# Kernel tuning notes

Hardware: AMD Instinct MI355X
Metric: run time of the kernel (lower is better)

## Reference

```python
import jax, jax.numpy as jnp
import numpy as np

N = 50000      # nodes
E = 800000     # edges (before self-loops)
D = 128        # hid_d
H = 8          # heads
C = D // H     # per-head channels
L = 3          # layers
SLOPE = 0.2    # GATv2 leaky_relu negative slope
EPS = 1e-5     # LayerNorm eps


def setup_inputs() -> dict:
    key = jax.random.key(0)
    ks = jax.random.split(key, 8)
    x = jax.random.normal(ks[0], (N, D), dtype=jnp.float32)
    ei = jax.random.randint(ks[1], (2, E), 0, N, dtype=jnp.int32)
    s = 1.0 / np.sqrt(D)
    Wl = jax.random.normal(ks[2], (L, D, D), dtype=jnp.float32) * s   # source transform per layer
    Wr = jax.random.normal(ks[3], (L, D, D), dtype=jnp.float32) * s   # target transform per layer
    att = jax.random.normal(ks[4], (L, H, C), dtype=jnp.float32) * (1.0 / np.sqrt(C))
    bias = jnp.zeros((L, D), dtype=jnp.float32)
    gamma = jnp.ones((L, D), dtype=jnp.float32)
    beta = jnp.zeros((L, D), dtype=jnp.float32)
    return {"x": x, "Wl": Wl, "Wr": Wr, "att": att, "bias": bias,
            "gamma": gamma, "beta": beta, "ei": ei}


def _layernorm(y, g, b):
    mu = jnp.mean(y, axis=-1, keepdims=True)
    var = jnp.mean(jnp.square(y - mu), axis=-1, keepdims=True)
    return (y - mu) * jax.lax.rsqrt(var + EPS) * g + b


def reference(x, Wl, Wr, att, bias, gamma, beta, ei):
    # append self-loops (PyG GATv2Conv default add_self_loops=True)
    loops = jnp.arange(N, dtype=ei.dtype)
    src = jnp.concatenate([ei[0], loops])  # [E+N]
    dst = jnp.concatenate([ei[1], loops])  # [E+N]
    h = x
    for l in range(L):
        xl = (h @ Wl[l]).reshape(N, H, C)   # source-side features
        xr = (h @ Wr[l]).reshape(N, H, C)   # target-side features
        feat = xl[src] + xr[dst]            # [E+N, H, C] per-edge gather
        logits = jnp.einsum('ehc,hc->eh', jax.nn.leaky_relu(feat, SLOPE), att[l])
        # segment softmax over incoming edges of each dst node
        m = jax.ops.segment_max(logits, dst, num_segments=N)
        ex = jnp.exp(logits - m[dst])
        denom = jax.ops.segment_sum(ex, dst, num_segments=N)
        alpha = ex / denom[dst]             # [E+N, H]
        msg = alpha[:, :, None] * xl[src]   # [E+N, H, C]
        out = jax.ops.segment_sum(msg, dst, num_segments=N).reshape(N, H * C) + bias[l]
        # wrapper: h = h + dropout(elu(norm(gat(h)))) ; dropout = identity (eval)
        h = h + jax.nn.elu(_layernorm(out, gamma[l], beta[l]))
    return h
```

## Files before the change

### kernel.cpp

```cpp
#include <hip/hip_runtime.h>
#include <hip/hip_fp16.h>
#include <math.h>

#define N_NODES 50000
#define N_EDGES 800000
#define D 128
#define L 3
#define SLOPE 0.2f
#define LN_EPS 1e-5f
#define ETOT (N_EDGES + N_NODES)
#define SCAN_BLOCKS ((N_NODES + 1023) / 1024)

typedef _Float16 half8 __attribute__((ext_vector_type(8)));
typedef _Float16 h4v  __attribute__((ext_vector_type(4)));
typedef _Float16 h2v  __attribute__((ext_vector_type(2)));
typedef float f32x4 __attribute__((ext_vector_type(4)));


__global__ void rank_hist_kernel(const int* __restrict__ ei, int* __restrict__ counts,
                                 int* __restrict__ rank) {
    int idx = blockIdx.x * blockDim.x + threadIdx.x;
    if (idx >= ETOT) return;
    int d = (idx < N_EDGES) ? ei[N_EDGES + idx] : (idx - N_EDGES);
    rank[idx] = atomicAdd(&counts[d], 1);
}

__global__ __launch_bounds__(1024) void scan1_kernel(const int* __restrict__ counts,
                                                     int* __restrict__ offsets,
                                                     int* __restrict__ bsum) {
    __shared__ int wsum[16];
    int tid = threadIdx.x;
    int lane = tid & 63, w = tid >> 6;
    int i = blockIdx.x * 1024 + tid;
    int v = (i < N_NODES) ? counts[i] : 0;
    int sc = v;
    #pragma unroll
    for (int off = 1; off < 64; off <<= 1) {
        int u = __shfl_up(sc, off);
        if (lane >= off) sc += u;
    }
    if (lane == 63) wsum[w] = sc;
    __syncthreads();
    if (w == 0) {
        int t2 = (lane < 16) ? wsum[lane] : 0;
        #pragma unroll
        for (int off = 1; off < 16; off <<= 1) {
            int u = __shfl_up(t2, off);
            if (lane >= off) t2 += u;
        }
        if (lane < 16) wsum[lane] = t2;
    }
    __syncthreads();
    int wpref = (w == 0) ? 0 : wsum[w - 1];
    if (i < N_NODES) offsets[i] = wpref + sc - v;
    if (tid == 0) bsum[blockIdx.x] = wsum[15];
}

__global__ __launch_bounds__(64) void scan2_kernel(const int* __restrict__ bsum,
                                                   int* __restrict__ bpre) {
    int lane = threadIdx.x;
    int v = (lane < SCAN_BLOCKS) ? bsum[lane] : 0;
    int sc = v;
    #pragma unroll
    for (int off = 1; off < 64; off <<= 1) {
        int u = __shfl_up(sc, off);
        if (lane >= off) sc += u;
    }
    if (lane < SCAN_BLOCKS) bpre[lane] = sc - v;
}

__global__ __launch_bounds__(1024) void scan3_kernel(int* __restrict__ offsets,
                                                     const int* __restrict__ bpre) {
    int i = blockIdx.x * 1024 + threadIdx.x;
    if (i < N_NODES) offsets[i] += bpre[blockIdx.x];
    if (i == 0) offsets[N_NODES] = ETOT;
}

__global__ void scatter_kernel(const int* __restrict__ ei, const int* __restrict__ offsets,
                               const int* __restrict__ rank,
                               unsigned short* __restrict__ sorted16) {
    int idx = blockIdx.x * blockDim.x + threadIdx.x;
    if (idx >= ETOT) return;
    int s, d;
    if (idx < N_EDGES) { s = ei[idx]; d = ei[N_EDGES + idx]; }
    else               { s = d = idx - N_EDGES; }
    sorted16[offsets[d] + rank[idx]] = (unsigned short)s;
}


__global__ __launch_bounds__(256) void wfrag_kernel(const float* __restrict__ Wl,
                                                    const float* __restrict__ Wr,
                                                    _Float16* __restrict__ Wfrag) {
    int u = blockIdx.x * 256 + threadIdx.x;
    if (u >= 3 * 4096) return;
    int lane = u & 63, nt = (u >> 6) & 7, kt = (u >> 9) & 3, y = (u >> 11) & 1, l = u >> 12;
    int r = lane & 15, q = lane >> 4;
    const float* W = (y ? Wr : Wl) + (size_t)l * D * D;
    half8 v;
    #pragma unroll
    for (int j = 0; j < 8; ++j)
        v[j] = (_Float16)W[(kt * 32 + q * 8 + j) * D + nt * 16 + r];
    *(half8*)&Wfrag[(size_t)u * 8] = v;
}


__global__ __launch_bounds__(256) void gemm_mfma_kernel(
        const float* __restrict__ h, const _Float16* __restrict__ WfragL,
        _Float16* __restrict__ xlh, _Float16* __restrict__ xrh) {
    __shared__ half8 Afrag[1024];
    int t = threadIdx.x;
    int row0 = blockIdx.x * 64;
    {
        int kt = t >> 6, q = (t >> 4) & 3, r = t & 15;
        int kc = kt * 4 + q;
        #pragma unroll
        for (int i = 0; i < 4; ++i) {
            int row = row0 + i * 16 + r;
            float4 f0 = make_float4(0.f, 0.f, 0.f, 0.f), f1 = f0;
            if (row < N_NODES) {
                const float* p = &h[(size_t)row * D + kc * 8];
                f0 = *(const float4*)p;
                f1 = *(const float4*)(p + 4);
            }
            half8 v;
            v[0] = (_Float16)f0.x; v[1] = (_Float16)f0.y;
            v[2] = (_Float16)f0.z; v[3] = (_Float16)f0.w;
            v[4] = (_Float16)f1.x; v[5] = (_Float16)f1.y;
            v[6] = (_Float16)f1.z; v[7] = (_Float16)f1.w;
            Afrag[i * 256 + t] = v;
        }
    }
    __syncthreads();
    int w = t >> 6, lane = t & 63;
    f32x4 acc[16];
    #pragma unroll
    for (int i = 0; i < 16; ++i) acc[i] = (f32x4){0.f, 0.f, 0.f, 0.f};
    #pragma unroll
    for (int kt = 0; kt < 4; ++kt) {
        half8 a = Afrag[(w * 4 + kt) * 64 + lane];
        #pragma unroll
        for (int y = 0; y < 2; ++y) {
            #pragma unroll
            for (int nt = 0; nt < 8; ++nt) {
                half8 b = *(const half8*)&WfragL[(size_t)(((y * 4 + kt) * 8 + nt) * 64 + lane) * 8];
                acc[y * 8 + nt] = __builtin_amdgcn_mfma_f32_16x16x32_f16(a, b, acc[y * 8 + nt], 0, 0, 0);
            }
        }
    }
    int rq = lane >> 4, rc = lane & 15;
    int rbase = row0 + w * 16 + rq * 4;
    #pragma unroll
    for (int y = 0; y < 2; ++y) {
        _Float16* out = y ? xrh : xlh;
        #pragma unroll
        for (int nt = 0; nt < 8; ++nt) {
            #pragma unroll
            for (int reg = 0; reg < 4; ++reg) {
                int row = rbase + reg;
                if (row < N_NODES)
                    out[(size_t)row * D + nt * 16 + rc] = (_Float16)acc[y * 8 + nt][reg];
            }
        }
    }
}


__device__ __forceinline__ float quad_reduce4(float p) {
    int t;
    t = __builtin_amdgcn_update_dpp(0, __float_as_int(p), 0xB1, 0xF, 0xF, true);
    p += __int_as_float(t);
    t = __builtin_amdgcn_update_dpp(0, __float_as_int(p), 0x4E, 0xF, 0xF, true);
    p += __int_as_float(t);
    return p;
}

__device__ __forceinline__ float logit4(h4v v, h2v xrA, h2v xrB, h2v attA, h2v attB,
                                        h2v slope2) {
    h2v v0; v0[0] = v[0]; v0[1] = v[1];
    h2v v1; v1[0] = v[2]; v1[1] = v[3];
    h2v f0 = v0 + xrA;
    h2v f1 = v1 + xrB;
    h2v lf0 = __builtin_elementwise_max(f0, f0 * slope2);
    h2v lf1 = __builtin_elementwise_max(f1, f1 * slope2);
    float p = __builtin_amdgcn_fdot2(lf0, attA, 0.f, false);
    return __builtin_amdgcn_fdot2(lf1, attB, p, false);
}

template<int KUN, bool MASK>
__device__ __forceinline__ void edge_block(
        int j, int idx_bp, unsigned off, unsigned laneoff, const char* xlb,
        h2v xrA, h2v xrB, h2v attA, h2v attB, h2v slope2, int cnt,
        float& s, float& a0, float& a1, float& a2, float& a3) {
    h4v vs[KUN];
    #pragma unroll
    for (int k = 0; k < KUN; ++k) {
        int o = __builtin_amdgcn_ds_bpermute(idx_bp + 4 * (j + k), (int)off);
        vs[k] = *(const h4v*)(xlb + ((unsigned)o + laneoff));
    }
    #pragma unroll
    for (int k = 0; k < KUN; ++k) {
        float p = logit4(vs[k], xrA, xrB, attA, attB, slope2);
        p = quad_reduce4(p);
        float e = __builtin_amdgcn_exp2f(p);
        if (MASK) e = (j + k < cnt) ? e : 0.f;
        s += e;
        a0 = fmaf(e, (float)vs[k][0], a0);
        a1 = fmaf(e, (float)vs[k][1], a1);
        a2 = fmaf(e, (float)vs[k][2], a2);
        a3 = fmaf(e, (float)vs[k][3], a3);
    }
}

__global__ __launch_bounds__(256) void gat_node_kernel(
        const _Float16* __restrict__ xlh, const _Float16* __restrict__ xrh,
        const int* __restrict__ offsets, const unsigned short* __restrict__ sorted16,
        const float* __restrict__ att_l, const float* __restrict__ bias_l,
        const float* __restrict__ gamma_l, const float* __restrict__ beta_l,
        const float* __restrict__ hin, float* __restrict__ hout) {
    int wid = (blockIdx.x * blockDim.x + threadIdx.x) >> 6;
    if (wid * 2 >= N_NODES) return;
    int lane = threadIdx.x & 63;
    int sub = lane >> 5, hl = lane & 31;
    int node = wid * 2 + sub;
    unsigned laneoff = hl * 8u;
    int idx_bp = sub << 7;

    h4v xr4 = *(const h4v*)&xrh[(size_t)node * D + hl * 4];
    h2v xrA; xrA[0] = xr4[0]; xrA[1] = xr4[1];
    h2v xrB; xrB[0] = xr4[2]; xrB[1] = xr4[3];
    float4 attf = *(const float4*)&att_l[hl * 4];
    h2v attA, attB, slope2;
    attA[0] = (_Float16)(attf.x * 1.44269504f);
    attA[1] = (_Float16)(attf.y * 1.44269504f);
    attB[0] = (_Float16)(attf.z * 1.44269504f);
    attB[1] = (_Float16)(attf.w * 1.44269504f);
    slope2[0] = (_Float16)SLOPE;
    slope2[1] = (_Float16)SLOPE;

    int beg = offsets[node], end = offsets[node + 1];
    int deg = end - beg;
    int degA = __builtin_amdgcn_readlane(deg, 0);
    int degB = __builtin_amdgcn_readlane(deg, 32);
    int degMax = degA > degB ? degA : degB;
    int degMin = degA < degB ? degA : degB;

    float s = 0.f;
    float acc0 = 0.f, acc1 = 0.f, acc2 = 0.f, acc3 = 0.f;
    const char* xlb = (const char*)xlh;

    for (int c0 = 0; c0 < degMax; c0 += 32) {
        int rem = deg - c0;
        int cnt = rem > 32 ? 32 : rem;
        int cl  = cnt > 0 ? (hl < cnt ? hl : cnt - 1) : 0;
        int pos = cnt > 0 ? beg + c0 + cl : beg;
        unsigned off = ((unsigned)sorted16[pos]) << 8;
        int jmax = degMax - c0; if (jmax > 32) jmax = 32;
        int nfull = degMin - c0; if (nfull > 32) nfull = 32; if (nfull < 0) nfull = 0;
        int j = 0;
        for (; j + 16 <= nfull; j += 16)
            edge_block<16, false>(j, idx_bp, off, laneoff, xlb, xrA, xrB,
                                  attA, attB, slope2, cnt, s, acc0, acc1, acc2, acc3);
        for (; j + 16 <= jmax; j += 16)
            edge_block<16, true>(j, idx_bp, off, laneoff, xlb, xrA, xrB,
                                 attA, attB, slope2, cnt, s, acc0, acc1, acc2, acc3);
        for (; j + 4 <= jmax; j += 4)
            edge_block<4, true>(j, idx_bp, off, laneoff, xlb, xrA, xrB,
                                attA, attB, slope2, cnt, s, acc0, acc1, acc2, acc3);
        for (; j < jmax; ++j)
            edge_block<1, true>(j, idx_bp, off, laneoff, xlb, xrA, xrB,
                                attA, attB, slope2, cnt, s, acc0, acc1, acc2, acc3);
    }

    float inv = 1.f / s;
    float4 bia = *(const float4*)&bias_l[hl * 4];
    float o0 = acc0 * inv + bia.x;
    float o1 = acc1 * inv + bia.y;
    float o2 = acc2 * inv + bia.z;
    float o3 = acc3 * inv + bia.w;
    float sum = (o0 + o1) + (o2 + o3);
    float sq  = (o0 * o0 + o1 * o1) + (o2 * o2 + o3 * o3);
    #pragma unroll
    for (int msk = 1; msk < 32; msk <<= 1) {
        sum += __shfl_xor(sum, msk);
        sq  += __shfl_xor(sq, msk);
    }
    float mu   = sum * (1.f / 128.f);
    float var  = sq * (1.f / 128.f) - mu * mu;
    float rstd = rsqrtf(var + LN_EPS);
    float4 gam = *(const float4*)&gamma_l[hl * 4];
    float4 bet = *(const float4*)&beta_l[hl * 4];
    float y0 = (o0 - mu) * rstd * gam.x + bet.x;
    float y1 = (o1 - mu) * rstd * gam.y + bet.y;
    float y2 = (o2 - mu) * rstd * gam.z + bet.z;
    float y3 = (o3 - mu) * rstd * gam.w + bet.w;
    y0 = y0 > 0.f ? y0 : __expf(y0) - 1.f;
    y1 = y1 > 0.f ? y1 : __expf(y1) - 1.f;
    y2 = y2 > 0.f ? y2 : __expf(y2) - 1.f;
    y3 = y3 > 0.f ? y3 : __expf(y3) - 1.f;
    size_t di = (size_t)node * D + hl * 4;
    float4 hv = *(const float4*)&hin[di];
    hv.x += y0; hv.y += y1; hv.z += y2; hv.w += y3;
    *(float4*)&hout[di] = hv;
}


extern "C" void kernel_launch(void* const* d_in, const int* in_sizes, int n_in,
                              void* d_out, int out_size, void* d_ws, size_t ws_size,
                              hipStream_t stream) {
    const float* x     = (const float*)d_in[0];
    const float* Wl    = (const float*)d_in[1];
    const float* Wr    = (const float*)d_in[2];
    const float* att   = (const float*)d_in[3];
    const float* bias  = (const float*)d_in[4];
    const float* gamma = (const float*)d_in[5];
    const float* beta  = (const float*)d_in[6];
    const int*   ei    = (const int*)d_in[7];
    float* h = (float*)d_out;

    char* ws = (char*)d_ws;
    _Float16* xlh = (_Float16*)ws;   ws += (size_t)N_NODES * D * sizeof(_Float16);
    _Float16* xrh = (_Float16*)ws;   ws += (size_t)N_NODES * D * sizeof(_Float16);
    _Float16* Wfrag = (_Float16*)ws; ws += (size_t)3 * 4096 * 8 * sizeof(_Float16);
    int* offsets = (int*)ws;         ws += (size_t)(N_NODES + 4) * sizeof(int);
    int* counts  = (int*)ws;         ws += (size_t)N_NODES * sizeof(int);
    int* bsum    = (int*)ws;         ws += 64 * sizeof(int);
    int* bpre    = (int*)ws;         ws += 64 * sizeof(int);
    int* rank    = (int*)ws;         ws += (size_t)ETOT * sizeof(int);
    unsigned short* sorted16 = (unsigned short*)ws;

    wfrag_kernel<<<48, 256, 0, stream>>>(Wl, Wr, Wfrag);
    (void)hipMemsetAsync(counts, 0, (size_t)N_NODES * sizeof(int), stream);
    rank_hist_kernel<<<(ETOT + 255) / 256, 256, 0, stream>>>(ei, counts, rank);
    scan1_kernel<<<SCAN_BLOCKS, 1024, 0, stream>>>(counts, offsets, bsum);
    scan2_kernel<<<1, 64, 0, stream>>>(bsum, bpre);
    scan3_kernel<<<SCAN_BLOCKS, 1024, 0, stream>>>(offsets, bpre);
    scatter_kernel<<<(ETOT + 255) / 256, 256, 0, stream>>>(ei, offsets, rank, sorted16);

    int gat_waves  = (N_NODES + 1) / 2;
    int gat_blocks = (gat_waves * 64 + 255) / 256;
    for (int l = 0; l < L; ++l) {
        const float* hin = (l == 0) ? x : h;
        gemm_mfma_kernel<<<(N_NODES + 63) / 64, 256, 0, stream>>>(
            hin, Wfrag + (size_t)l * 4096 * 8, xlh, xrh);
        gat_node_kernel<<<gat_blocks, 256, 0, stream>>>(
            xlh, xrh, offsets, sorted16,
            att + (size_t)l * D, bias + (size_t)l * D,
            gamma + (size_t)l * D, beta + (size_t)l * D, hin, h);
    }
}
```

Before: 336.6 us.

## Process four nodes per wave with 8-wide lanes and degree-sorted node order

The GAT aggregation kernel now assigns 16 lanes per node, with each lane handling 8 channels through half8 loads, so a wave covers four nodes. This also shortens the head reduction to a single DPP step. A counting sort by in-degree, built from a histogram, a scan and a scatter, produces a node permutation so that the four nodes sharing a wave have similar degrees, which cuts masked iterations from divergent degrees. In exchange it adds three small preprocessing kernels and a memset, and writes to hout in permuted, less coalesced order.

```diff
diff --git a/kernel.cpp b/kernel.cpp
--- a/kernel.cpp
+++ b/kernel.cpp
@@ -85,6 +85,43 @@
     if (idx < N_EDGES) { s = ei[idx]; d = ei[N_EDGES + idx]; }
     else               { s = d = idx - N_EDGES; }
     sorted16[offsets[d] + rank[idx]] = (unsigned short)s;
+}
+
+
+__global__ void deg_hist_kernel(const int* __restrict__ counts, int* __restrict__ hist) {
+    int i = blockIdx.x * blockDim.x + threadIdx.x;
+    if (i >= N_NODES) return;
+    int d = counts[i]; if (d > 255) d = 255;
+    atomicAdd(&hist[d], 1);
+}
+
+__global__ __launch_bounds__(64) void deg_scan_kernel(const int* __restrict__ hist,
+                                                      int* __restrict__ histoff) {
+    int lane = threadIdx.x;
+    int4 v = ((const int4*)hist)[lane];
+    int t = v.x + v.y + v.z + v.w;
+    int sc = t;
+    #pragma unroll
+    for (int off = 1; off < 64; off <<= 1) {
+        int u = __shfl_up(sc, off);
+        if (lane >= off) sc += u;
+    }
+    int base = sc - t;
+    int4 o;
+    o.x = base;
+    o.y = base + v.x;
+    o.z = base + v.x + v.y;
+    o.w = base + v.x + v.y + v.z;
+    ((int4*)histoff)[lane] = o;
+}
+
+__global__ void deg_scatter_kernel(const int* __restrict__ counts, int* __restrict__ histoff,
+                                   int* __restrict__ perm) {
+    int i = blockIdx.x * blockDim.x + threadIdx.x;
+    if (i >= N_NODES) return;
+    int d = counts[i]; if (d > 255) d = 255;
+    int pos = atomicAdd(&histoff[d], 1);
+    perm[pos] = i;
 }
 
 
@@ -165,142 +202,158 @@
 }
 
 
-__device__ __forceinline__ float quad_reduce4(float p) {
+__device__ __forceinline__ float pair_reduce2(float p) {
     int t;
     t = __builtin_amdgcn_update_dpp(0, __float_as_int(p), 0xB1, 0xF, 0xF, true);
     p += __int_as_float(t);
-    t = __builtin_amdgcn_update_dpp(0, __float_as_int(p), 0x4E, 0xF, 0xF, true);
-    p += __int_as_float(t);
     return p;
 }
 
-__device__ __forceinline__ float logit4(h4v v, h2v xrA, h2v xrB, h2v attA, h2v attB,
-                                        h2v slope2) {
-    h2v v0; v0[0] = v[0]; v0[1] = v[1];
-    h2v v1; v1[0] = v[2]; v1[1] = v[3];
-    h2v f0 = v0 + xrA;
-    h2v f1 = v1 + xrB;
-    h2v lf0 = __builtin_elementwise_max(f0, f0 * slope2);
-    h2v lf1 = __builtin_elementwise_max(f1, f1 * slope2);
-    float p = __builtin_amdgcn_fdot2(lf0, attA, 0.f, false);
-    return __builtin_amdgcn_fdot2(lf1, attB, p, false);
+__device__ __forceinline__ float logit8(half8 v, half8 xr, const h2v* att4, h2v slope2) {
+    float p = 0.f;
+    #pragma unroll
+    for (int i = 0; i < 4; ++i) {
+        h2v a; a[0] = v[2 * i];  a[1] = v[2 * i + 1];
+        h2v b; b[0] = xr[2 * i]; b[1] = xr[2 * i + 1];
+        h2v f  = a + b;
+        h2v lf = __builtin_elementwise_max(f, f * slope2);
+        p = __builtin_amdgcn_fdot2(lf, att4[i], p, false);
+    }
+    return p;
 }
 
 template<int KUN, bool MASK>
 __device__ __forceinline__ void edge_block(
         int j, int idx_bp, unsigned off, unsigned laneoff, const char* xlb,
-        h2v xrA, h2v xrB, h2v attA, h2v attB, h2v slope2, int cnt,
-        float& s, float& a0, float& a1, float& a2, float& a3) {
-    h4v vs[KUN];
+        half8 xr8, const h2v* att4, h2v slope2, int cnt,
+        float& s, float* acc) {
+    half8 vs[KUN];
     #pragma unroll
     for (int k = 0; k < KUN; ++k) {
         int o = __builtin_amdgcn_ds_bpermute(idx_bp + 4 * (j + k), (int)off);
-        vs[k] = *(const h4v*)(xlb + ((unsigned)o + laneoff));
+        vs[k] = *(const half8*)(xlb + ((unsigned)o + laneoff));
     }
     #pragma unroll
     for (int k = 0; k < KUN; ++k) {
-        float p = logit4(vs[k], xrA, xrB, attA, attB, slope2);
-        p = quad_reduce4(p);
+        float p = logit8(vs[k], xr8, att4, slope2);
+        p = pair_reduce2(p);
         float e = __builtin_amdgcn_exp2f(p);
         if (MASK) e = (j + k < cnt) ? e : 0.f;
         s += e;
-        a0 = fmaf(e, (float)vs[k][0], a0);
-        a1 = fmaf(e, (float)vs[k][1], a1);
-        a2 = fmaf(e, (float)vs[k][2], a2);
-        a3 = fmaf(e, (float)vs[k][3], a3);
+        #pragma unroll
+        for (int i = 0; i < 8; ++i)
+            acc[i] = fmaf(e, (float)vs[k][i], acc[i]);
     }
 }
 
 __global__ __launch_bounds__(256) void gat_node_kernel(
         const _Float16* __restrict__ xlh, const _Float16* __restrict__ xrh,
         const int* __restrict__ offsets, const unsigned short* __restrict__ sorted16,
+        const int* __restrict__ perm,
         const float* __restrict__ att_l, const float* __restrict__ bias_l,
         const float* __restrict__ gamma_l, const float* __restrict__ beta_l,
         const float* __restrict__ hin, float* __restrict__ hout) {
     int wid = (blockIdx.x * blockDim.x + threadIdx.x) >> 6;
-    if (wid * 2 >= N_NODES) return;
+    if (wid * 4 >= N_NODES) return;
     int lane = threadIdx.x & 63;
-    int sub = lane >> 5, hl = lane & 31;
-    int node = wid * 2 + sub;
-    unsigned laneoff = hl * 8u;
-    int idx_bp = sub << 7;
-
-    h4v xr4 = *(const h4v*)&xrh[(size_t)node * D + hl * 4];
-    h2v xrA; xrA[0] = xr4[0]; xrA[1] = xr4[1];
-    h2v xrB; xrB[0] = xr4[2]; xrB[1] = xr4[3];
-    float4 attf = *(const float4*)&att_l[hl * 4];
-    h2v attA, attB, slope2;
-    attA[0] = (_Float16)(attf.x * 1.44269504f);
-    attA[1] = (_Float16)(attf.y * 1.44269504f);
-    attB[0] = (_Float16)(attf.z * 1.44269504f);
-    attB[1] = (_Float16)(attf.w * 1.44269504f);
+    int g = lane >> 4, hl = lane & 15;
+    int node = perm[wid * 4 + g];
+    unsigned laneoff = hl * 16u;
+    int idx_bp = g << 6;
+
+    half8 xr8 = *(const half8*)&xrh[(size_t)node * D + hl * 8];
+    float4 af0 = *(const float4*)&att_l[hl * 8];
+    float4 af1 = *(const float4*)&att_l[hl * 8 + 4];
+    h2v att4[4], slope2;
+    att4[0][0] = (_Float16)(af0.x * 1.44269504f);
+    att4[0][1] = (_Float16)(af0.y * 1.44269504f);
+    att4[1][0] = (_Float16)(af0.z * 1.44269504f);
+    att4[1][1] = (_Float16)(af0.w * 1.44269504f);
+    att4[2][0] = (_Float16)(af1.x * 1.44269504f);
+    att4[2][1] = (_Float16)(af1.y * 1.44269504f);
+    att4[3][0] = (_Float16)(af1.z * 1.44269504f);
+    att4[3][1] = (_Float16)(af1.w * 1.44269504f);
     slope2[0] = (_Float16)SLOPE;
     slope2[1] = (_Float16)SLOPE;
 
     int beg = offsets[node], end = offsets[node + 1];
     int deg = end - beg;
-    int degA = __builtin_amdgcn_readlane(deg, 0);
-    int degB = __builtin_amdgcn_readlane(deg, 32);
-    int degMax = degA > degB ? degA : degB;
-    int degMin = degA < degB ? degA : degB;
+    int d0 = __builtin_amdgcn_readlane(deg, 0);
+    int d1 = __builtin_amdgcn_readlane(deg, 16);
+    int d2 = __builtin_amdgcn_readlane(deg, 32);
+    int d3 = __builtin_amdgcn_readlane(deg, 48);
+    int m01 = d0 > d1 ? d0 : d1, m23 = d2 > d3 ? d2 : d3;
+    int degMax = m01 > m23 ? m01 : m23;
+    int n01 = d0 < d1 ? d0 : d1, n23 = d2 < d3 ? d2 : d3;
+    int degMin = n01 < n23 ? n01 : n23;
 
     float s = 0.f;
-    float acc0 = 0.f, acc1 = 0.f, acc2 = 0.f, acc3 = 0.f;
+    float acc[8] = {0.f, 0.f, 0.f, 0.f, 0.f, 0.f, 0.f, 0.f};
     const char* xlb = (const char*)xlh;
 
-    for (int c0 = 0; c0 < degMax; c0 += 32) {
+    for (int c0 = 0; c0 < degMax; c0 += 16) {
         int rem = deg - c0;
-        int cnt = rem > 32 ? 32 : rem;
+        int cnt = rem > 16 ? 16 : rem;
         int cl  = cnt > 0 ? (hl < cnt ? hl : cnt - 1) : 0;
         int pos = cnt > 0 ? beg + c0 + cl : beg;
         unsigned off = ((unsigned)sorted16[pos]) << 8;
-        int jmax = degMax - c0; if (jmax > 32) jmax = 32;
-        int nfull = degMin - c0; if (nfull > 32) nfull = 32; if (nfull < 0) nfull = 0;
+        int jmax = degMax - c0; if (jmax > 16) jmax = 16;
+        int nfull = degMin - c0; if (nfull > 16) nfull = 16; if (nfull < 0) nfull = 0;
         int j = 0;
-        for (; j + 16 <= nfull; j += 16)
-            edge_block<16, false>(j, idx_bp, off, laneoff, xlb, xrA, xrB,
-                                  attA, attB, slope2, cnt, s, acc0, acc1, acc2, acc3);
-        for (; j + 16 <= jmax; j += 16)
-            edge_block<16, true>(j, idx_bp, off, laneoff, xlb, xrA, xrB,
-                                 attA, attB, slope2, cnt, s, acc0, acc1, acc2, acc3);
+        for (; j + 8 <= nfull; j += 8)
+            edge_block<8, false>(j, idx_bp, off, laneoff, xlb, xr8, att4, slope2,
+                                 cnt, s, acc);
+        for (; j + 4 <= nfull; j += 4)
+            edge_block<4, false>(j, idx_bp, off, laneoff, xlb, xr8, att4, slope2,
+                                 cnt, s, acc);
         for (; j + 4 <= jmax; j += 4)
-            edge_block<4, true>(j, idx_bp, off, laneoff, xlb, xrA, xrB,
-                                attA, attB, slope2, cnt, s, acc0, acc1, acc2, acc3);
+            edge_block<4, true>(j, idx_bp, off, laneoff, xlb, xr8, att4, slope2,
+                                cnt, s, acc);
         for (; j < jmax; ++j)
-            edge_block<1, true>(j, idx_bp, off, laneoff, xlb, xrA, xrB,
-                                attA, attB, slope2, cnt, s, acc0, acc1, acc2, acc3);
+            edge_block<1, true>(j, idx_bp, off, laneoff, xlb, xr8, att4, slope2,
+                                cnt, s, acc);
     }
 
     float inv = 1.f / s;
-    float4 bia = *(const float4*)&bias_l[hl * 4];
-    float o0 = acc0 * inv + bia.x;
-    float o1 = acc1 * inv + bia.y;
-    float o2 = acc2 * inv + bia.z;
-    float o3 = acc3 * inv + bia.w;
-    float sum = (o0 + o1) + (o2 + o3);
-    float sq  = (o0 * o0 + o1 * o1) + (o2 * o2 + o3 * o3);
-    #pragma unroll
-    for (int msk = 1; msk < 32; msk <<= 1) {
+    float4 b0 = *(const float4*)&bias_l[hl * 8];
+    float4 b1 = *(const float4*)&bias_l[hl * 8 + 4];
+    float o[8];
+    o[0] = acc[0] * inv + b0.x; o[1] = acc[1] * inv + b0.y;
+    o[2] = acc[2] * inv + b0.z; o[3] = acc[3] * inv + b0.w;
+    o[4] = acc[4] * inv + b1.x; o[5] = acc[5] * inv + b1.y;
+    o[6] = acc[6] * inv + b1.z; o[7] = acc[7] * inv + b1.w;
+    float sum = ((o[0] + o[1]) + (o[2] + o[3])) + ((o[4] + o[5]) + (o[6] + o[7]));
+    float sq  = ((o[0] * o[0] + o[1] * o[1]) + (o[2] * o[2] + o[3] * o[3]))
+              + ((o[4] * o[4] + o[5] * o[5]) + (o[6] * o[6] + o[7] * o[7]));
+    #pragma unroll
+    for (int msk = 1; msk < 16; msk <<= 1) {
         sum += __shfl_xor(sum, msk);
         sq  += __shfl_xor(sq, msk);
     }
     float mu   = sum * (1.f / 128.f);
     float var  = sq * (1.f / 128.f) - mu * mu;
     float rstd = rsqrtf(var + LN_EPS);
-    float4 gam = *(const float4*)&gamma_l[hl * 4];
-    float4 bet = *(const float4*)&beta_l[hl * 4];
-    float y0 = (o0 - mu) * rstd * gam.x + bet.x;
-    float y1 = (o1 - mu) * rstd * gam.y + bet.y;
-    float y2 = (o2 - mu) * rstd * gam.z + bet.z;
-    float y3 = (o3 - mu) * rstd * gam.w + bet.w;
-    y0 = y0 > 0.f ? y0 : __expf(y0) - 1.f;
-    y1 = y1 > 0.f ? y1 : __expf(y1) - 1.f;
-    y2 = y2 > 0.f ? y2 : __expf(y2) - 1.f;
-    y3 = y3 > 0.f ? y3 : __expf(y3) - 1.f;
-    size_t di = (size_t)node * D + hl * 4;
-    float4 hv = *(const float4*)&hin[di];
-    hv.x += y0; hv.y += y1; hv.z += y2; hv.w += y3;
-    *(float4*)&hout[di] = hv;
+    float4 g0 = *(const float4*)&gamma_l[hl * 8];
+    float4 g1 = *(const float4*)&gamma_l[hl * 8 + 4];
+    float4 e0 = *(const float4*)&beta_l[hl * 8];
+    float4 e1 = *(const float4*)&beta_l[hl * 8 + 4];
+    float gam[8] = {g0.x, g0.y, g0.z, g0.w, g1.x, g1.y, g1.z, g1.w};
+    float bet[8] = {e0.x, e0.y, e0.z, e0.w, e1.x, e1.y, e1.z, e1.w};
+    size_t di = (size_t)node * D + hl * 8;
+    float4 h0 = *(const float4*)&hin[di];
+    float4 h1 = *(const float4*)&hin[di + 4];
+    float hv[8] = {h0.x, h0.y, h0.z, h0.w, h1.x, h1.y, h1.z, h1.w};
+    float y[8];
+    #pragma unroll
+    for (int i = 0; i < 8; ++i) {
+        float t = (o[i] - mu) * rstd * gam[i] + bet[i];
+        t = t > 0.f ? t : __expf(t) - 1.f;
+        y[i] = hv[i] + t;
+    }
+    float4 w0 = make_float4(y[0], y[1], y[2], y[3]);
+    float4 w1 = make_float4(y[4], y[5], y[6], y[7]);
+    *(float4*)&hout[di]     = w0;
+    *(float4*)&hout[di + 4] = w1;
 }
 
 
@@ -325,25 +378,32 @@
     int* counts  = (int*)ws;         ws += (size_t)N_NODES * sizeof(int);
     int* bsum    = (int*)ws;         ws += 64 * sizeof(int);
     int* bpre    = (int*)ws;         ws += 64 * sizeof(int);
+    int* hist    = (int*)ws;         ws += 256 * sizeof(int);
+    int* histoff = (int*)ws;         ws += 256 * sizeof(int);
+    int* perm    = (int*)ws;         ws += (size_t)N_NODES * sizeof(int);
     int* rank    = (int*)ws;         ws += (size_t)ETOT * sizeof(int);
     unsigned short* sorted16 = (unsigned short*)ws;
 
     wfrag_kernel<<<48, 256, 0, stream>>>(Wl, Wr, Wfrag);
     (void)hipMemsetAsync(counts, 0, (size_t)N_NODES * sizeof(int), stream);
+    (void)hipMemsetAsync(hist, 0, 256 * sizeof(int), stream);
     rank_hist_kernel<<<(ETOT + 255) / 256, 256, 0, stream>>>(ei, counts, rank);
     scan1_kernel<<<SCAN_BLOCKS, 1024, 0, stream>>>(counts, offsets, bsum);
     scan2_kernel<<<1, 64, 0, stream>>>(bsum, bpre);
     scan3_kernel<<<SCAN_BLOCKS, 1024, 0, stream>>>(offsets, bpre);
     scatter_kernel<<<(ETOT + 255) / 256, 256, 0, stream>>>(ei, offsets, rank, sorted16);
-
-    int gat_waves  = (N_NODES + 1) / 2;
+    deg_hist_kernel<<<(N_NODES + 255) / 256, 256, 0, stream>>>(counts, hist);
+    deg_scan_kernel<<<1, 64, 0, stream>>>(hist, histoff);
+    deg_scatter_kernel<<<(N_NODES + 255) / 256, 256, 0, stream>>>(counts, histoff, perm);
+
+    int gat_waves  = (N_NODES + 3) / 4;
     int gat_blocks = (gat_waves * 64 + 255) / 256;
     for (int l = 0; l < L; ++l) {
         const float* hin = (l == 0) ? x : h;
         gemm_mfma_kernel<<<(N_NODES + 63) / 64, 256, 0, stream>>>(
             hin, Wfrag + (size_t)l * 4096 * 8, xlh, xrh);
         gat_node_kernel<<<gat_blocks, 256, 0, stream>>>(
-            xlh, xrh, offsets, sorted16,
+            xlh, xrh, offsets, sorted16, perm,
             att + (size_t)l * D, bias + (size_t)l * D,
             gamma + (size_t)l * D, beta + (size_t)l * D, hin, h);
     }
```

Result: slower. 623.3 us (+85.2%).
